# Optimization experiments

Hardware: AMD Instinct MI355X
Metric: run time of the kernel (lower is better)

Reference implementation:

```python
import jax, jax.numpy as jnp
import numpy as np

B, T, D, H = 2, 2048, 1024, 16
HS = D // H  # head_size = 64
EPS = 1e-5


def layer_norm(x, g, b):
    mu = jnp.mean(x, axis=-1, keepdims=True)
    var = jnp.var(x, axis=-1, keepdims=True)
    return (x - mu) * jax.lax.rsqrt(var + EPS) * g + b


def setup_inputs() -> dict:
    key = jax.random.key(0)
    ks = jax.random.split(key, 12)
    s_attn = 1.0 / np.sqrt(D)
    s_ff1 = 1.0 / np.sqrt(D)
    s_ff2 = 1.0 / np.sqrt(4 * D)
    return {
        "x": jax.random.normal(ks[0], (B, T, D), jnp.float32),
        "Wq": jax.random.normal(ks[1], (H, D, HS), jnp.float32) * s_attn,
        "Wk": jax.random.normal(ks[2], (H, D, HS), jnp.float32) * s_attn,
        "Wv": jax.random.normal(ks[3], (H, D, HS), jnp.float32) * s_attn,
        "Wo": jax.random.normal(ks[4], (H * HS, D), jnp.float32) * (1.0 / np.sqrt(H * HS)),
        "bo": jnp.zeros((D,), jnp.float32),
        "W1": jax.random.normal(ks[5], (D, 4 * D), jnp.float32) * s_ff1,
        "b1": jnp.zeros((4 * D,), jnp.float32),
        "W2": jax.random.normal(ks[6], (4 * D, D), jnp.float32) * s_ff2,
        "b2": jnp.zeros((D,), jnp.float32),
        "ln1_g": jnp.ones((D,), jnp.float32),
        "ln1_b": jnp.zeros((D,), jnp.float32),
        "ln2_g": jnp.ones((D,), jnp.float32),
        "ln2_b": jnp.zeros((D,), jnp.float32),
    }


def reference(x, Wq, Wk, Wv, Wo, bo, W1, b1, W2, b2, ln1_g, ln1_b, ln2_g, ln2_b):
    # --- self-attention on ln1(x) ---
    h = layer_norm(x, ln1_g, ln1_b)
    Q = jnp.einsum('bsd,hdk->bhsk', h, Wq)
    K = jnp.einsum('bsd,hdk->bhsk', h, Wk)
    V = jnp.einsum('bsd,hdk->bhsk', h, Wv)
    scores = jnp.einsum('bhqk,bhsk->bhqs', Q, K) * (HS ** -0.5)
    attn = jax.nn.softmax(scores, axis=-1)  # [B,H,T,T] non-causal, as in source
    out = jnp.einsum('bhqs,bhsk->bhqk', attn, V)
    out = out.transpose(0, 2, 1, 3).reshape(B, T, H * HS)  # concat heads
    sa = out @ Wo + bo
    x = x + sa
    # --- feed-forward on ln2(x) ---
    h2 = layer_norm(x, ln2_g, ln2_b)
    ff = jax.nn.relu(h2 @ W1 + b1) @ W2 + b2
    return x + ff
```

## Files before the change

### kernel.cpp

```cpp
#include <hip/hip_runtime.h>
#include <cstdint>
#include <cmath>

typedef __bf16 bf16;
typedef __bf16 bf16x8 __attribute__((ext_vector_type(8)));
typedef __bf16 bf16x4 __attribute__((ext_vector_type(4)));
typedef __bf16 bf16x2 __attribute__((ext_vector_type(2)));
typedef float  f32x4  __attribute__((ext_vector_type(4)));

#define B_   2
#define T_   2048
#define D_   1024
#define H_   16
#define HS_  64
#define NTOK (B_ * T_)

typedef __attribute__((address_space(1))) uint8_t* gp1_t;
typedef __attribute__((address_space(3))) uint8_t* lp3_t;
__device__ __forceinline__ void gl_lds16(const void* g, void* l) {
    __builtin_amdgcn_global_load_lds((gp1_t)(uintptr_t)g,
                                     (lp3_t)(uint32_t)(uintptr_t)l,
                                     16, 0, 0);
}

__device__ __forceinline__ f32x4 mfma16(bf16x8 a, bf16x8 b, f32x4 c) {
    return __builtin_amdgcn_mfma_f32_16x16x32_bf16(a, b, c, 0, 0, 0);
}

__device__ __forceinline__ uint32_t pk2(float lo, float hi) {
    bf16x2 t; t[0] = (bf16)lo; t[1] = (bf16)hi;
    return __builtin_bit_cast(uint32_t, t);
}
__device__ __forceinline__ void pl32(uint32_t& a, uint32_t& b) {
    asm("v_permlane32_swap_b32 %0, %1" : "+v"(a), "+v"(b));
}
__device__ __forceinline__ void pl16(uint32_t& a, uint32_t& b) {
    asm("v_permlane16_swap_b32 %0, %1" : "+v"(a), "+v"(b));
}

__global__ void tcast(const float* __restrict__ in, bf16* __restrict__ out,
                      int R, int C) {
    __shared__ float t[32][33];
    const int c0 = blockIdx.x * 32, r0 = blockIdx.y * 32;
    for (int i = 0; i < 4; i++) {
        int r = threadIdx.y + i * 8;
        t[r][threadIdx.x] = in[(size_t)(r0 + r) * C + c0 + threadIdx.x];
    }
    __syncthreads();
    for (int i = 0; i < 4; i++) {
        int rr = threadIdx.y + i * 8;
        out[(size_t)(c0 + rr) * R + r0 + threadIdx.x] = (bf16)t[threadIdx.x][rr];
    }
}

__global__ void qkv_pack(const float* __restrict__ Wq, const float* __restrict__ Wk,
                         const float* __restrict__ Wv, bf16* __restrict__ out) {
    const int z = blockIdx.z;
    const int qkv = z >> 4;
    const float* in = (qkv == 0 ? Wq : qkv == 1 ? Wk : Wv) + (size_t)(z & 15) * D_ * HS_;
    bf16* o = out + (size_t)z * HS_ * D_;
    __shared__ float t[32][33];
    const int c0 = blockIdx.x * 32, r0 = blockIdx.y * 32;
    for (int i = 0; i < 4; i++) {
        int r = threadIdx.y + i * 8;
        t[r][threadIdx.x] = in[(size_t)(r0 + r) * HS_ + c0 + threadIdx.x];
    }
    __syncthreads();
    for (int i = 0; i < 4; i++) {
        int rr = threadIdx.y + i * 8;
        o[(size_t)(c0 + rr) * D_ + r0 + threadIdx.x] = (bf16)t[threadIdx.x][rr];
    }
}

__global__ __launch_bounds__(256) void ln_kernel(const float* __restrict__ x,
                                                 const float* __restrict__ g,
                                                 const float* __restrict__ b,
                                                 bf16* __restrict__ out) {
    const int row = blockIdx.x;
    const int tid = threadIdx.x;
    const float4 v = ((const float4*)(x + (size_t)row * 1024))[tid];
    float s  = v.x + v.y + v.z + v.w;
    float s2 = v.x * v.x + v.y * v.y + v.z * v.z + v.w * v.w;
    for (int m = 1; m < 64; m <<= 1) {
        s  += __shfl_xor(s, m);
        s2 += __shfl_xor(s2, m);
    }
    __shared__ float rs[4], rq[4];
    const int lane = tid & 63, wv = tid >> 6;
    if (lane == 0) { rs[wv] = s; rq[wv] = s2; }
    __syncthreads();
    s  = rs[0] + rs[1] + rs[2] + rs[3];
    s2 = rq[0] + rq[1] + rq[2] + rq[3];
    const float mu   = s * (1.f / 1024.f);
    const float var  = s2 * (1.f / 1024.f) - mu * mu;
    const float rstd = rsqrtf(var + 1e-5f);
    const float4 gg = ((const float4*)g)[tid];
    const float4 bb = ((const float4*)b)[tid];
    bf16x4 o;
    o[0] = (bf16)((v.x - mu) * rstd * gg.x + bb.x);
    o[1] = (bf16)((v.y - mu) * rstd * gg.y + bb.y);
    o[2] = (bf16)((v.z - mu) * rstd * gg.z + bb.z);
    o[3] = (bf16)((v.w - mu) * rstd * gg.w + bb.w);
    *(bf16x4*)(out + (size_t)row * 1024 + tid * 4) = o;
}

__global__ __launch_bounds__(256) void combine4(const float* __restrict__ p0,
                                                const float* __restrict__ p1,
                                                const float* __restrict__ p2,
                                                const float* __restrict__ p3,
                                                const float* __restrict__ resid,
                                                const float* __restrict__ bias,
                                                float* __restrict__ out) {
    const int i4 = blockIdx.x * 256 + threadIdx.x;
    const float4 a = ((const float4*)p0)[i4];
    const float4 b = ((const float4*)p1)[i4];
    const float4 c = ((const float4*)p2)[i4];
    const float4 d = ((const float4*)p3)[i4];
    const float4 r = ((const float4*)resid)[i4];
    const float4 bb = ((const float4*)bias)[i4 & 255];
    float4 o;
    o.x = a.x + b.x + c.x + d.x + r.x + bb.x;
    o.y = a.y + b.y + c.y + d.y + r.y + bb.y;
    o.z = a.z + b.z + c.z + d.z + r.z + bb.z;
    o.w = a.w + b.w + c.w + d.w + r.w + bb.w;
    ((float4*)out)[i4] = o;
}

template <int BIAS, int RELU, int RES, int OUTBF16>
__global__ __launch_bounds__(256, 2) void gemm_bt(
    const bf16* __restrict__ A, const bf16* __restrict__ Bt,
    const float* __restrict__ bias, const float* __restrict__ resid,
    void* __restrict__ Cout, int M, int N, int K) {
    __shared__ __align__(16) bf16 As[2][128 * 32];
    __shared__ __align__(16) bf16 Bs[2][128 * 32];
    const int tid  = threadIdx.x;
    const int lane = tid & 63, w = tid >> 6;
    const int quad = lane >> 4, l15 = lane & 15;
    const int m0 = blockIdx.y * 128, n0 = blockIdx.x * 128;
    const int wm = (w & 1) * 64, wn = (w >> 1) * 64;

    f32x4 acc[4][4];
    for (int i = 0; i < 4; i++)
        for (int j = 0; j < 4; j++) acc[i][j] = f32x4{0.f, 0.f, 0.f, 0.f};

    const int arow = lane >> 2;
    const int acol = (lane & 3) * 8;
    const int c0 = w * 2, c1 = w * 2 + 1;

    for (int kt = 0; kt < K; kt += 64) {
        gl_lds16(A  + (size_t)(m0 + c0 * 16 + arow) * K + kt + acol,      &As[0][c0 * 512]);
        gl_lds16(A  + (size_t)(m0 + c1 * 16 + arow) * K + kt + acol,      &As[0][c1 * 512]);
        gl_lds16(A  + (size_t)(m0 + c0 * 16 + arow) * K + kt + 32 + acol, &As[1][c0 * 512]);
        gl_lds16(A  + (size_t)(m0 + c1 * 16 + arow) * K + kt + 32 + acol, &As[1][c1 * 512]);
        gl_lds16(Bt + (size_t)(n0 + c0 * 16 + arow) * K + kt + acol,      &Bs[0][c0 * 512]);
        gl_lds16(Bt + (size_t)(n0 + c1 * 16 + arow) * K + kt + acol,      &Bs[0][c1 * 512]);
        gl_lds16(Bt + (size_t)(n0 + c0 * 16 + arow) * K + kt + 32 + acol, &Bs[1][c0 * 512]);
        gl_lds16(Bt + (size_t)(n0 + c1 * 16 + arow) * K + kt + 32 + acol, &Bs[1][c1 * 512]);
        __syncthreads();
        for (int kh = 0; kh < 2; kh++) {
            bf16x8 af[4], bfr[4];
            for (int mi = 0; mi < 4; mi++)
                af[mi] = *(const bf16x8*)&As[kh][(wm + mi * 16 + l15) * 32 + quad * 8];
            for (int ni = 0; ni < 4; ni++)
                bfr[ni] = *(const bf16x8*)&Bs[kh][(wn + ni * 16 + l15) * 32 + quad * 8];
            for (int mi = 0; mi < 4; mi++)
                for (int ni = 0; ni < 4; ni++)
                    acc[mi][ni] = mfma16(af[mi], bfr[ni], acc[mi][ni]);
        }
        __syncthreads();
    }

    for (int mi = 0; mi < 4; mi++) {
        for (int ni = 0; ni < 4; ni++) {
            const int colb = n0 + wn + ni * 16 + l15;
            const float bv = BIAS ? bias[colb] : 0.f;
            for (int r = 0; r < 4; r++) {
                const int row = m0 + wm + mi * 16 + quad * 4 + r;
                float v = acc[mi][ni][r] + bv;
                if (RELU) v = fmaxf(v, 0.f);
                if (RES)  v += resid[(size_t)row * N + colb];
                if (OUTBF16) ((bf16*)Cout)[(size_t)row * N + colb] = (bf16)v;
                else         ((float*)Cout)[(size_t)row * N + colb] = v;
            }
        }
    }
}

template <int BIAS, int RELU, int VTP, int PARTIAL>
__global__ __launch_bounds__(512, 2) void gemm256(
    const bf16* __restrict__ A, const bf16* __restrict__ Bt,
    const float* __restrict__ bias, void* __restrict__ Cout,
    bf16* __restrict__ Vt, float* __restrict__ P0, float* __restrict__ P1,
    int M, int N, int K) {
    __shared__ __align__(16) bf16 Asub[4][256 * 32];
    __shared__ __align__(16) bf16 Bsub[4][256 * 32];
    const int tid  = threadIdx.x;
    const int lane = tid & 63, w = tid >> 6;
    const int wr = w >> 2, wc = w & 3;
    const int quad = lane >> 4, l15 = lane & 15;
    const int m0 = blockIdx.y * 256, n0 = blockIdx.x * 256;
    const int kpb = PARTIAL ? (K / (int)gridDim.z) : K;
    const int k0  = PARTIAL ? (int)blockIdx.z * kpb : 0;
    const int S   = kpb / 32;

    const int slog = (((lane & 3) ^ ((lane >> 3) & 3)) * 8);
    const int crow = lane >> 2;
    const bf16* gA0 = A  + (size_t)(m0 + 32 * w + crow)      * K + k0 + slog;
    const bf16* gA1 = A  + (size_t)(m0 + 32 * w + 16 + crow) * K + k0 + slog;
    const bf16* gB0 = Bt + (size_t)(n0 + 32 * w + crow)      * K + k0 + slog;
    const bf16* gB1 = Bt + (size_t)(n0 + 32 * w + 16 + crow) * K + k0 + slog;

    for (int t = 0; t < 3; t++) {
        gl_lds16(gA0, &Asub[t][(32 * w) * 32]);
        gl_lds16(gA1, &Asub[t][(32 * w + 16) * 32]);
        gl_lds16(gB0, &Bsub[t][(32 * w) * 32]);
        gl_lds16(gB1, &Bsub[t][(32 * w + 16) * 32]);
        gA0 += 32; gA1 += 32; gB0 += 32; gB1 += 32;
    }

    f32x4 acc[8][4];
#pragma unroll
    for (int i = 0; i < 8; i++)
#pragma unroll
        for (int j = 0; j < 4; j++) acc[i][j] = f32x4{0.f, 0.f, 0.f, 0.f};

    const int swz = (quad ^ ((l15 >> 1) & 3)) * 8;
    const int aof = (wr * 128 + l15) * 32 + swz;
    const int bof = (wc * 64 + l15) * 32 + swz;

    asm volatile("s_waitcnt vmcnt(8)" ::: "memory");
    __builtin_amdgcn_sched_barrier(0);
    __builtin_amdgcn_s_barrier();

    for (int s = 0; s < S; s++) {
        const bf16* Ab = &Asub[s & 3][0];
        const bf16* Bb = &Bsub[s & 3][0];
        const int pb = (s + 3) & 3;
        bf16x8 af[4], bfr[4];
#pragma unroll
        for (int f = 0; f < 4; f++) af[f] = *(const bf16x8*)&Ab[aof + f * 512];
#pragma unroll
        for (int n = 0; n < 4; n++) bfr[n] = *(const bf16x8*)&Bb[bof + n * 512];
        if (s + 3 < S) {
            gl_lds16(gA0, &Asub[pb][(32 * w) * 32]);
            gl_lds16(gA1, &Asub[pb][(32 * w + 16) * 32]);
            gA0 += 32; gA1 += 32;
        }
        __builtin_amdgcn_sched_barrier(0);
        __builtin_amdgcn_s_barrier();
        asm volatile("s_waitcnt lgkmcnt(0)" ::: "memory");
        __builtin_amdgcn_sched_barrier(0);
        __builtin_amdgcn_s_setprio(1);
#pragma unroll
        for (int f = 0; f < 4; f++)
#pragma unroll
            for (int n = 0; n < 4; n++)
                acc[f][n] = mfma16(af[f], bfr[n], acc[f][n]);
        __builtin_amdgcn_s_setprio(0);
        __builtin_amdgcn_sched_barrier(0);
        __builtin_amdgcn_s_barrier();
#pragma unroll
        for (int f = 0; f < 4; f++) af[f] = *(const bf16x8*)&Ab[aof + 2048 + f * 512];
        if (s + 3 < S) {
            gl_lds16(gB0, &Bsub[pb][(32 * w) * 32]);
            gl_lds16(gB1, &Bsub[pb][(32 * w + 16) * 32]);
            gB0 += 32; gB1 += 32;
        }
        __builtin_amdgcn_sched_barrier(0);
        __builtin_amdgcn_s_barrier();
        asm volatile("s_waitcnt lgkmcnt(0)" ::: "memory");
        __builtin_amdgcn_sched_barrier(0);
        __builtin_amdgcn_s_setprio(1);
#pragma unroll
        for (int f = 0; f < 4; f++)
#pragma unroll
            for (int n = 0; n < 4; n++)
                acc[4 + f][n] = mfma16(af[f], bfr[n], acc[4 + f][n]);
        __builtin_amdgcn_s_setprio(0);
        __builtin_amdgcn_sched_barrier(0);
        if (s <= S - 4)      asm volatile("s_waitcnt vmcnt(8)" ::: "memory");
        else if (s == S - 3) asm volatile("s_waitcnt vmcnt(4)" ::: "memory");
        else if (s == S - 2) asm volatile("s_waitcnt vmcnt(0)" ::: "memory");
        __builtin_amdgcn_s_barrier();
    }

#pragma unroll
    for (int mi = 0; mi < 8; mi++) {
#pragma unroll
        for (int ni = 0; ni < 4; ni++) {
            const int colb = n0 + wc * 64 + ni * 16 + l15;
            const int row0 = m0 + wr * 128 + (mi >> 2) * 64 + (mi & 3) * 16 + quad * 4;
            if (VTP && colb >= 2048) {
                const int h = (colb - 2048) >> 6, hs = (colb - 2048) & 63;
                const int b = row0 >> 11;
                bf16x4 p4;
                p4[0] = (bf16)acc[mi][ni][0];
                p4[1] = (bf16)acc[mi][ni][1];
                p4[2] = (bf16)acc[mi][ni][2];
                p4[3] = (bf16)acc[mi][ni][3];
                *(bf16x4*)&Vt[((size_t)(b * 16 + h) * 64 + hs) * T_ + (row0 & 2047)] = p4;
                continue;
            }
            if (PARTIAL) {
                float* Cz = ((int)blockIdx.z < 2 ? P0 : P1) + (size_t)(blockIdx.z & 1) * M * N;
                for (int r = 0; r < 4; r++)
                    Cz[(size_t)(row0 + r) * N + colb] = acc[mi][ni][r];
            } else {
                const float bv = BIAS ? bias[colb] : 0.f;
                for (int r = 0; r < 4; r++) {
                    float v = acc[mi][ni][r] + bv;
                    if (RELU) v = fmaxf(v, 0.f);
                    ((bf16*)Cout)[(size_t)(row0 + r) * N + colb] = (bf16)v;
                }
            }
        }
    }
}

#define LSTR 68
#define NJ   (T_ / 64)
__global__ __launch_bounds__(256, 2) void flash_attn(const bf16* __restrict__ QKV,
                                                     const bf16* __restrict__ Vt,
                                                     bf16* __restrict__ attn_out) {
    const int bh = blockIdx.y, b = bh >> 4, h = bh & 15;
    const int q0 = blockIdx.x * 128;
    const int tid = threadIdx.x, lane = tid & 63, w = tid >> 6;
    const int quad = lane >> 4, l15 = lane & 15;
    __shared__ __align__(16) bf16 Ks[2][64 * LSTR];
    __shared__ __align__(16) bf16 Vs[2][64 * LSTR];
    const bf16* Qb = QKV + (size_t)b * T_ * 3072 + h * 64;
    const bf16* Kb = QKV + (size_t)b * T_ * 3072 + 1024 + h * 64;
    const bf16* Vb = Vt  + (size_t)bh * HS_ * T_;

    const float sc = 0.125f * 1.44269504088896f;
    const int sr = tid >> 2, scc = (tid & 3) * 16;

    bf16x8 QA[2][2];
    for (int qnt = 0; qnt < 2; qnt++) {
        const size_t row = (size_t)(q0 + w * 32 + qnt * 16 + l15) * 3072;
        for (int kk = 0; kk < 2; kk++) {
            bf16x8 q = *(const bf16x8*)&Qb[row + kk * 32 + quad * 8];
            for (int i = 0; i < 8; i++) q[i] = (bf16)((float)q[i] * sc);
            QA[qnt][kk] = q;
        }
    }

    bf16x8 ones8;
    for (int i = 0; i < 8; i++) ones8[i] = (bf16)1.0f;

    f32x4 O[2][4], lacc[2];
    for (int mi = 0; mi < 2; mi++) {
        lacc[mi] = f32x4{0.f, 0.f, 0.f, 0.f};
        for (int n = 0; n < 4; n++) O[mi][n] = f32x4{0.f, 0.f, 0.f, 0.f};
    }

    *(bf16x8*)&Ks[0][sr * LSTR + scc]     = *(const bf16x8*)&Kb[(size_t)sr * 3072 + scc];
    *(bf16x8*)&Ks[0][sr * LSTR + scc + 8] = *(const bf16x8*)&Kb[(size_t)sr * 3072 + scc + 8];
    *(bf16x8*)&Vs[0][sr * LSTR + scc]     = *(const bf16x8*)&Vb[(size_t)sr * T_ + scc];
    *(bf16x8*)&Vs[0][sr * LSTR + scc + 8] = *(const bf16x8*)&Vb[(size_t)sr * T_ + scc + 8];
    __syncthreads();

    bf16x8 k0, k1, v0, v1;
    for (int j = 0; j < NJ; j++) {
        const int buf = j & 1;
        if (j + 1 < NJ) {
            const int s1 = (j + 1) * 64;
            k0 = *(const bf16x8*)&Kb[(size_t)(s1 + sr) * 3072 + scc];
            k1 = *(const bf16x8*)&Kb[(size_t)(s1 + sr) * 3072 + scc + 8];
            v0 = *(const bf16x8*)&Vb[(size_t)sr * T_ + s1 + scc];
            v1 = *(const bf16x8*)&Vb[(size_t)sr * T_ + s1 + scc + 8];
        }
        bf16x8 KB[4][2];
#pragma unroll
        for (int smt = 0; smt < 4; smt++)
#pragma unroll
            for (int kk = 0; kk < 2; kk++)
                KB[smt][kk] = *(const bf16x8*)&Ks[buf][(smt * 16 + l15) * LSTR + kk * 32 + quad * 8];

        bf16x8 PA[2][2];
#pragma unroll
        for (int qnt = 0; qnt < 2; qnt++) {
            f32x4 ST[4];
#pragma unroll
            for (int smt = 0; smt < 4; smt++) ST[smt] = f32x4{0.f, 0.f, 0.f, 0.f};
            __builtin_amdgcn_s_setprio(1);
#pragma unroll
            for (int kk = 0; kk < 2; kk++)
#pragma unroll
                for (int smt = 0; smt < 4; smt++)
                    ST[smt] = mfma16(KB[smt][kk], QA[qnt][kk], ST[smt]);
            __builtin_amdgcn_s_setprio(0);
            uint32_t w00 = pk2(__builtin_amdgcn_exp2f(ST[0][0]), __builtin_amdgcn_exp2f(ST[0][1]));
            uint32_t w01 = pk2(__builtin_amdgcn_exp2f(ST[0][2]), __builtin_amdgcn_exp2f(ST[0][3]));
            uint32_t w10 = pk2(__builtin_amdgcn_exp2f(ST[1][0]), __builtin_amdgcn_exp2f(ST[1][1]));
            uint32_t w11 = pk2(__builtin_amdgcn_exp2f(ST[1][2]), __builtin_amdgcn_exp2f(ST[1][3]));
            uint32_t w20 = pk2(__builtin_amdgcn_exp2f(ST[2][0]), __builtin_amdgcn_exp2f(ST[2][1]));
            uint32_t w21 = pk2(__builtin_amdgcn_exp2f(ST[2][2]), __builtin_amdgcn_exp2f(ST[2][3]));
            uint32_t w30 = pk2(__builtin_amdgcn_exp2f(ST[3][0]), __builtin_amdgcn_exp2f(ST[3][1]));
            uint32_t w31 = pk2(__builtin_amdgcn_exp2f(ST[3][2]), __builtin_amdgcn_exp2f(ST[3][3]));
            pl32(w00, w10); pl16(w00, w10);
            pl32(w01, w11); pl16(w01, w11);
            pl32(w20, w30); pl16(w20, w30);
            pl32(w21, w31); pl16(w21, w31);
            union { uint32_t u[4]; bf16x8 v; } pa0, pa1;
            pa0.u[0] = w00; pa0.u[1] = w01; pa0.u[2] = w10; pa0.u[3] = w11;
            pa1.u[0] = w20; pa1.u[1] = w21; pa1.u[2] = w30; pa1.u[3] = w31;
            PA[qnt][0] = pa0.v;
            PA[qnt][1] = pa1.v;
        }
        bf16x8 VB[4][2];
#pragma unroll
        for (int n = 0; n < 4; n++)
#pragma unroll
            for (int kk = 0; kk < 2; kk++)
                VB[n][kk] = *(const bf16x8*)&Vs[buf][(n * 16 + l15) * LSTR + kk * 32 + quad * 8];
        __builtin_amdgcn_s_setprio(1);
#pragma unroll
        for (int mi = 0; mi < 2; mi++) {
            const bf16x8 PA0 = PA[mi][0];
            const bf16x8 PA1 = PA[mi][1];
#pragma unroll
            for (int n = 0; n < 4; n++) {
                O[mi][n] = mfma16(PA0, VB[n][0], O[mi][n]);
                O[mi][n] = mfma16(PA1, VB[n][1], O[mi][n]);
            }
            lacc[mi] = mfma16(PA0, ones8, lacc[mi]);
            lacc[mi] = mfma16(PA1, ones8, lacc[mi]);
        }
        __builtin_amdgcn_s_setprio(0);
        if (j + 1 < NJ) {
            *(bf16x8*)&Ks[buf ^ 1][sr * LSTR + scc]     = k0;
            *(bf16x8*)&Ks[buf ^ 1][sr * LSTR + scc + 8] = k1;
            *(bf16x8*)&Vs[buf ^ 1][sr * LSTR + scc]     = v0;
            *(bf16x8*)&Vs[buf ^ 1][sr * LSTR + scc + 8] = v1;
        }
        __syncthreads();
    }

    for (int mi = 0; mi < 2; mi++) {
        for (int r = 0; r < 4; r++) {
            const float inv = 1.f / lacc[mi][r];
            const size_t tok = (size_t)b * T_ + q0 + w * 32 + mi * 16 + quad * 4 + r;
            for (int n = 0; n < 4; n++)
                attn_out[tok * 1024 + h * 64 + n * 16 + l15] = (bf16)(O[mi][n][r] * inv);
        }
    }
}

extern "C" void kernel_launch(void* const* d_in, const int* in_sizes, int n_in,
                              void* d_out, int out_size, void* d_ws, size_t ws_size,
                              hipStream_t stream) {
    const float* x   = (const float*)d_in[0];
    const float* Wq  = (const float*)d_in[1];
    const float* Wk  = (const float*)d_in[2];
    const float* Wv  = (const float*)d_in[3];
    const float* Wo  = (const float*)d_in[4];
    const float* bo  = (const float*)d_in[5];
    const float* W1  = (const float*)d_in[6];
    const float* b1  = (const float*)d_in[7];
    const float* W2  = (const float*)d_in[8];
    const float* b2  = (const float*)d_in[9];
    const float* g1  = (const float*)d_in[10];
    const float* be1 = (const float*)d_in[11];
    const float* g2  = (const float*)d_in[12];
    const float* be2 = (const float*)d_in[13];

    char* ws = (char*)d_ws;
    const size_t MB = 1ull << 20;
    bf16*  WqkvT = (bf16*)(ws);
    bf16*  WoT   = (bf16*)(ws + 6  * MB);
    bf16*  W1T   = (bf16*)(ws + 8  * MB);
    bf16*  W2T   = (bf16*)(ws + 16 * MB);
    bf16*  hbuf  = (bf16*)(ws + 24 * MB);
    bf16*  QKV   = (bf16*)(ws + 32 * MB);
    bf16*  Vt    = (bf16*)(ws + 56 * MB);
    bf16*  attn  = (bf16*)(ws + 64 * MB);
    float* x2    = (float*)(ws + 72 * MB);
    bf16*  ff1   = (bf16*)(ws + 32 * MB);
    float* partA = (float*)(ws);
    float* partB = (float*)(ws + 88 * MB);
    float* out   = (float*)d_out;

    dim3 tb(32, 8);
    qkv_pack<<<dim3(2, 32, 48), tb, 0, stream>>>(Wq, Wk, Wv, WqkvT);
    tcast<<<dim3(32, 32),  tb, 0, stream>>>(Wo, WoT, 1024, 1024);
    tcast<<<dim3(128, 32), tb, 0, stream>>>(W1, W1T, 1024, 4096);
    tcast<<<dim3(32, 128), tb, 0, stream>>>(W2, W2T, 4096, 1024);
    ln_kernel<<<NTOK, 256, 0, stream>>>(x, g1, be1, hbuf);
    gemm256<0, 0, 1, 0><<<dim3(12, 16), 512, 0, stream>>>(
        hbuf, WqkvT, nullptr, QKV, Vt, nullptr, nullptr, NTOK, 3072, 1024);
    flash_attn<<<dim3(T_ / 128, B_ * H_), 256, 0, stream>>>(QKV, Vt, attn);
    gemm_bt<1, 0, 1, 0><<<dim3(8, 32), 256, 0, stream>>>(attn, WoT, bo, x, x2, NTOK, 1024, 1024);
    ln_kernel<<<NTOK, 256, 0, stream>>>(x2, g2, be2, hbuf);
    gemm256<1, 1, 0, 0><<<dim3(16, 16), 512, 0, stream>>>(
        hbuf, W1T, b1, ff1, nullptr, nullptr, nullptr, NTOK, 4096, 1024);
    gemm256<0, 0, 0, 1><<<dim3(4, 16, 4), 512, 0, stream>>>(
        ff1, W2T, nullptr, nullptr, nullptr, partA, partB, NTOK, 1024, 4096);
    combine4<<<NTOK, 256, 0, stream>>>(partA, partA + (size_t)NTOK * 1024,
                                       partB, partB + (size_t)NTOK * 1024,
                                       x2, b2, out);
}
```

Measured before the change: 341.1 us.

## Make flash attention single-wave with register-direct K/V loads; use 128-tile QKV GEMM

Flash attention drops shared-memory K/V staging and block barriers. Each 64-thread block now handles 32 queries and loads K and V fragments straight from global memory into registers, prefetching the next tile while the current one is computed. The QKV projection moves from the 256-tile GEMM to the 128-tile gemm_bt, which gains a V-transpose epilogue, giving more blocks. The aim is to remove LDS traffic and sync stalls and raise block count, at the cost of each wave re-reading K/V from global memory/L2 with less reuse across waves.

```diff
diff --git a/kernel.cpp b/kernel.cpp
--- a/kernel.cpp
+++ b/kernel.cpp
@@ -126,11 +126,11 @@
     ((float4*)out)[i4] = o;
 }
 
-template <int BIAS, int RELU, int RES, int OUTBF16>
+template <int BIAS, int RELU, int RES, int OUTBF16, int VTP = 0>
 __global__ __launch_bounds__(256, 2) void gemm_bt(
     const bf16* __restrict__ A, const bf16* __restrict__ Bt,
     const float* __restrict__ bias, const float* __restrict__ resid,
-    void* __restrict__ Cout, int M, int N, int K) {
+    void* __restrict__ Cout, bf16* __restrict__ Vt, int M, int N, int K) {
     __shared__ __align__(16) bf16 As[2][128 * 32];
     __shared__ __align__(16) bf16 Bs[2][128 * 32];
     const int tid  = threadIdx.x;
@@ -173,6 +173,18 @@
     for (int mi = 0; mi < 4; mi++) {
         for (int ni = 0; ni < 4; ni++) {
             const int colb = n0 + wn + ni * 16 + l15;
+            if (VTP && colb >= 2048) {
+                const int h = (colb - 2048) >> 6, hs = (colb - 2048) & 63;
+                const int row0 = m0 + wm + mi * 16 + quad * 4;
+                const int b = row0 >> 11;
+                bf16x4 p4;
+                p4[0] = (bf16)acc[mi][ni][0];
+                p4[1] = (bf16)acc[mi][ni][1];
+                p4[2] = (bf16)acc[mi][ni][2];
+                p4[3] = (bf16)acc[mi][ni][3];
+                *(bf16x4*)&Vt[((size_t)(b * 16 + h) * 64 + hs) * T_ + (row0 & 2047)] = p4;
+                continue;
+            }
             const float bv = BIAS ? bias[colb] : 0.f;
             for (int r = 0; r < 4; r++) {
                 const int row = m0 + wm + mi * 16 + quad * 4 + r;
@@ -317,29 +329,28 @@
     }
 }
 
-#define LSTR 68
 #define NJ   (T_ / 64)
-__global__ __launch_bounds__(256, 2) void flash_attn(const bf16* __restrict__ QKV,
-                                                     const bf16* __restrict__ Vt,
-                                                     bf16* __restrict__ attn_out) {
+__global__ __launch_bounds__(64, 2) void flash_attn(const bf16* __restrict__ QKV,
+                                                    const bf16* __restrict__ Vt,
+                                                    bf16* __restrict__ attn_out) {
     const int bh = blockIdx.y, b = bh >> 4, h = bh & 15;
-    const int q0 = blockIdx.x * 128;
-    const int tid = threadIdx.x, lane = tid & 63, w = tid >> 6;
+    const int q0 = blockIdx.x * 32;
+    const int lane = threadIdx.x;
     const int quad = lane >> 4, l15 = lane & 15;
-    __shared__ __align__(16) bf16 Ks[2][64 * LSTR];
-    __shared__ __align__(16) bf16 Vs[2][64 * LSTR];
     const bf16* Qb = QKV + (size_t)b * T_ * 3072 + h * 64;
     const bf16* Kb = QKV + (size_t)b * T_ * 3072 + 1024 + h * 64;
     const bf16* Vb = Vt  + (size_t)bh * HS_ * T_;
 
     const float sc = 0.125f * 1.44269504088896f;
-    const int sr = tid >> 2, scc = (tid & 3) * 16;
+    const int koff = quad * 8;
 
     bf16x8 QA[2][2];
+#pragma unroll
     for (int qnt = 0; qnt < 2; qnt++) {
-        const size_t row = (size_t)(q0 + w * 32 + qnt * 16 + l15) * 3072;
+        const size_t row = (size_t)(q0 + qnt * 16 + l15) * 3072;
+#pragma unroll
         for (int kk = 0; kk < 2; kk++) {
-            bf16x8 q = *(const bf16x8*)&Qb[row + kk * 32 + quad * 8];
+            bf16x8 q = *(const bf16x8*)&Qb[row + kk * 32 + koff];
             for (int i = 0; i < 8; i++) q[i] = (bf16)((float)q[i] * sc);
             QA[qnt][kk] = q;
         }
@@ -349,55 +360,58 @@
     for (int i = 0; i < 8; i++) ones8[i] = (bf16)1.0f;
 
     f32x4 O[2][4], lacc[2];
+#pragma unroll
     for (int mi = 0; mi < 2; mi++) {
         lacc[mi] = f32x4{0.f, 0.f, 0.f, 0.f};
         for (int n = 0; n < 4; n++) O[mi][n] = f32x4{0.f, 0.f, 0.f, 0.f};
     }
 
-    *(bf16x8*)&Ks[0][sr * LSTR + scc]     = *(const bf16x8*)&Kb[(size_t)sr * 3072 + scc];
-    *(bf16x8*)&Ks[0][sr * LSTR + scc + 8] = *(const bf16x8*)&Kb[(size_t)sr * 3072 + scc + 8];
-    *(bf16x8*)&Vs[0][sr * LSTR + scc]     = *(const bf16x8*)&Vb[(size_t)sr * T_ + scc];
-    *(bf16x8*)&Vs[0][sr * LSTR + scc + 8] = *(const bf16x8*)&Vb[(size_t)sr * T_ + scc + 8];
-    __syncthreads();
-
-    bf16x8 k0, k1, v0, v1;
+    bf16x8 KB[4][2], VB[4][2];
+#pragma unroll
+    for (int smt = 0; smt < 4; smt++)
+#pragma unroll
+        for (int kk = 0; kk < 2; kk++)
+            KB[smt][kk] = *(const bf16x8*)&Kb[(size_t)(smt * 16 + l15) * 3072 + kk * 32 + koff];
+#pragma unroll
+    for (int n = 0; n < 4; n++)
+#pragma unroll
+        for (int kk = 0; kk < 2; kk++)
+            VB[n][kk] = *(const bf16x8*)&Vb[(size_t)(n * 16 + l15) * T_ + kk * 32 + koff];
+
     for (int j = 0; j < NJ; j++) {
-        const int buf = j & 1;
+        f32x4 ST[2][4];
+#pragma unroll
+        for (int qnt = 0; qnt < 2; qnt++)
+#pragma unroll
+            for (int smt = 0; smt < 4; smt++) ST[qnt][smt] = f32x4{0.f, 0.f, 0.f, 0.f};
+        __builtin_amdgcn_s_setprio(1);
+#pragma unroll
+        for (int kk = 0; kk < 2; kk++)
+#pragma unroll
+            for (int qnt = 0; qnt < 2; qnt++)
+#pragma unroll
+                for (int smt = 0; smt < 4; smt++)
+                    ST[qnt][smt] = mfma16(KB[smt][kk], QA[qnt][kk], ST[qnt][smt]);
+        __builtin_amdgcn_s_setprio(0);
         if (j + 1 < NJ) {
-            const int s1 = (j + 1) * 64;
-            k0 = *(const bf16x8*)&Kb[(size_t)(s1 + sr) * 3072 + scc];
-            k1 = *(const bf16x8*)&Kb[(size_t)(s1 + sr) * 3072 + scc + 8];
-            v0 = *(const bf16x8*)&Vb[(size_t)sr * T_ + s1 + scc];
-            v1 = *(const bf16x8*)&Vb[(size_t)sr * T_ + s1 + scc + 8];
-        }
-        bf16x8 KB[4][2];
-#pragma unroll
-        for (int smt = 0; smt < 4; smt++)
-#pragma unroll
-            for (int kk = 0; kk < 2; kk++)
-                KB[smt][kk] = *(const bf16x8*)&Ks[buf][(smt * 16 + l15) * LSTR + kk * 32 + quad * 8];
-
+            const size_t s1 = (size_t)(j + 1) * 64;
+#pragma unroll
+            for (int smt = 0; smt < 4; smt++)
+#pragma unroll
+                for (int kk = 0; kk < 2; kk++)
+                    KB[smt][kk] = *(const bf16x8*)&Kb[(s1 + smt * 16 + l15) * 3072 + kk * 32 + koff];
+        }
         bf16x8 PA[2][2];
 #pragma unroll
         for (int qnt = 0; qnt < 2; qnt++) {
-            f32x4 ST[4];
-#pragma unroll
-            for (int smt = 0; smt < 4; smt++) ST[smt] = f32x4{0.f, 0.f, 0.f, 0.f};
-            __builtin_amdgcn_s_setprio(1);
-#pragma unroll
-            for (int kk = 0; kk < 2; kk++)
-#pragma unroll
-                for (int smt = 0; smt < 4; smt++)
-                    ST[smt] = mfma16(KB[smt][kk], QA[qnt][kk], ST[smt]);
-            __builtin_amdgcn_s_setprio(0);
-            uint32_t w00 = pk2(__builtin_amdgcn_exp2f(ST[0][0]), __builtin_amdgcn_exp2f(ST[0][1]));
-            uint32_t w01 = pk2(__builtin_amdgcn_exp2f(ST[0][2]), __builtin_amdgcn_exp2f(ST[0][3]));
-            uint32_t w10 = pk2(__builtin_amdgcn_exp2f(ST[1][0]), __builtin_amdgcn_exp2f(ST[1][1]));
-            uint32_t w11 = pk2(__builtin_amdgcn_exp2f(ST[1][2]), __builtin_amdgcn_exp2f(ST[1][3]));
-            uint32_t w20 = pk2(__builtin_amdgcn_exp2f(ST[2][0]), __builtin_amdgcn_exp2f(ST[2][1]));
-            uint32_t w21 = pk2(__builtin_amdgcn_exp2f(ST[2][2]), __builtin_amdgcn_exp2f(ST[2][3]));
-            uint32_t w30 = pk2(__builtin_amdgcn_exp2f(ST[3][0]), __builtin_amdgcn_exp2f(ST[3][1]));
-            uint32_t w31 = pk2(__builtin_amdgcn_exp2f(ST[3][2]), __builtin_amdgcn_exp2f(ST[3][3]));
+            uint32_t w00 = pk2(__builtin_amdgcn_exp2f(ST[qnt][0][0]), __builtin_amdgcn_exp2f(ST[qnt][0][1]));
+            uint32_t w01 = pk2(__builtin_amdgcn_exp2f(ST[qnt][0][2]), __builtin_amdgcn_exp2f(ST[qnt][0][3]));
+            uint32_t w10 = pk2(__builtin_amdgcn_exp2f(ST[qnt][1][0]), __builtin_amdgcn_exp2f(ST[qnt][1][1]));
+            uint32_t w11 = pk2(__builtin_amdgcn_exp2f(ST[qnt][1][2]), __builtin_amdgcn_exp2f(ST[qnt][1][3]));
+            uint32_t w20 = pk2(__builtin_amdgcn_exp2f(ST[qnt][2][0]), __builtin_amdgcn_exp2f(ST[qnt][2][1]));
+            uint32_t w21 = pk2(__builtin_amdgcn_exp2f(ST[qnt][2][2]), __builtin_amdgcn_exp2f(ST[qnt][2][3]));
+            uint32_t w30 = pk2(__builtin_amdgcn_exp2f(ST[qnt][3][0]), __builtin_amdgcn_exp2f(ST[qnt][3][1]));
+            uint32_t w31 = pk2(__builtin_amdgcn_exp2f(ST[qnt][3][2]), __builtin_amdgcn_exp2f(ST[qnt][3][3]));
             pl32(w00, w10); pl16(w00, w10);
             pl32(w01, w11); pl16(w01, w11);
             pl32(w20, w30); pl16(w20, w30);
@@ -408,12 +422,6 @@
             PA[qnt][0] = pa0.v;
             PA[qnt][1] = pa1.v;
         }
-        bf16x8 VB[4][2];
-#pragma unroll
-        for (int n = 0; n < 4; n++)
-#pragma unroll
-            for (int kk = 0; kk < 2; kk++)
-                VB[n][kk] = *(const bf16x8*)&Vs[buf][(n * 16 + l15) * LSTR + kk * 32 + quad * 8];
         __builtin_amdgcn_s_setprio(1);
 #pragma unroll
         for (int mi = 0; mi < 2; mi++) {
@@ -429,18 +437,20 @@
         }
         __builtin_amdgcn_s_setprio(0);
         if (j + 1 < NJ) {
-            *(bf16x8*)&Ks[buf ^ 1][sr * LSTR + scc]     = k0;
-            *(bf16x8*)&Ks[buf ^ 1][sr * LSTR + scc + 8] = k1;
-            *(bf16x8*)&Vs[buf ^ 1][sr * LSTR + scc]     = v0;
-            *(bf16x8*)&Vs[buf ^ 1][sr * LSTR + scc + 8] = v1;
-        }
-        __syncthreads();
-    }
-
+            const int s1 = (j + 1) * 64;
+#pragma unroll
+            for (int n = 0; n < 4; n++)
+#pragma unroll
+                for (int kk = 0; kk < 2; kk++)
+                    VB[n][kk] = *(const bf16x8*)&Vb[(size_t)(n * 16 + l15) * T_ + s1 + kk * 32 + koff];
+        }
+    }
+
+#pragma unroll
     for (int mi = 0; mi < 2; mi++) {
         for (int r = 0; r < 4; r++) {
             const float inv = 1.f / lacc[mi][r];
-            const size_t tok = (size_t)b * T_ + q0 + w * 32 + mi * 16 + quad * 4 + r;
+            const size_t tok = (size_t)b * T_ + q0 + mi * 16 + quad * 4 + r;
             for (int n = 0; n < 4; n++)
                 attn_out[tok * 1024 + h * 64 + n * 16 + l15] = (bf16)(O[mi][n][r] * inv);
         }
@@ -487,10 +497,11 @@
     tcast<<<dim3(128, 32), tb, 0, stream>>>(W1, W1T, 1024, 4096);
     tcast<<<dim3(32, 128), tb, 0, stream>>>(W2, W2T, 4096, 1024);
     ln_kernel<<<NTOK, 256, 0, stream>>>(x, g1, be1, hbuf);
-    gemm256<0, 0, 1, 0><<<dim3(12, 16), 512, 0, stream>>>(
-        hbuf, WqkvT, nullptr, QKV, Vt, nullptr, nullptr, NTOK, 3072, 1024);
-    flash_attn<<<dim3(T_ / 128, B_ * H_), 256, 0, stream>>>(QKV, Vt, attn);
-    gemm_bt<1, 0, 1, 0><<<dim3(8, 32), 256, 0, stream>>>(attn, WoT, bo, x, x2, NTOK, 1024, 1024);
+    gemm_bt<0, 0, 0, 1, 1><<<dim3(24, 32), 256, 0, stream>>>(
+        hbuf, WqkvT, nullptr, nullptr, QKV, Vt, NTOK, 3072, 1024);
+    flash_attn<<<dim3(T_ / 32, B_ * H_), 64, 0, stream>>>(QKV, Vt, attn);
+    gemm_bt<1, 0, 1, 0><<<dim3(8, 32), 256, 0, stream>>>(
+        attn, WoT, bo, x, x2, nullptr, NTOK, 1024, 1024);
     ln_kernel<<<NTOK, 256, 0, stream>>>(x2, g2, be2, hbuf);
     gemm256<1, 1, 0, 0><<<dim3(16, 16), 512, 0, stream>>>(
         hbuf, W1T, b1, ff1, nullptr, nullptr, nullptr, NTOK, 4096, 1024);
```

Result: slower. 411.2 us (+20.6%).

## Use 512-thread flash attention blocks with one 16-row query tile per wave

Applied to the files above, without the earlier changes.

Flash attention blocks grow from 4 to 8 waves, and each wave now handles 16 query rows instead of 32, so the 128-row block tile is kept. Per-thread register state drops (QA, O and lacc are halved) and the launch bounds target higher occupancy. K/V tile loads are spread across 512 threads, one 16-byte load each. In exchange, every K/V LDS fragment is read by twice as many waves for the same MFMA work, and each barrier now synchronises more waves.

```diff
diff --git a/kernel.cpp b/kernel.cpp
--- a/kernel.cpp
+++ b/kernel.cpp
@@ -319,7 +319,7 @@
 
 #define LSTR 68
 #define NJ   (T_ / 64)
-__global__ __launch_bounds__(256, 2) void flash_attn(const bf16* __restrict__ QKV,
+__global__ __launch_bounds__(512, 4) void flash_attn(const bf16* __restrict__ QKV,
                                                      const bf16* __restrict__ Vt,
                                                      bf16* __restrict__ attn_out) {
     const int bh = blockIdx.y, b = bh >> 4, h = bh & 15;
@@ -333,42 +333,38 @@
     const bf16* Vb = Vt  + (size_t)bh * HS_ * T_;
 
     const float sc = 0.125f * 1.44269504088896f;
-    const int sr = tid >> 2, scc = (tid & 3) * 16;
-
-    bf16x8 QA[2][2];
-    for (int qnt = 0; qnt < 2; qnt++) {
-        const size_t row = (size_t)(q0 + w * 32 + qnt * 16 + l15) * 3072;
+    const int sr = tid >> 3, scc = (tid & 7) * 8;
+
+    bf16x8 QA[2];
+    {
+        const size_t row = (size_t)(q0 + w * 16 + l15) * 3072;
+#pragma unroll
         for (int kk = 0; kk < 2; kk++) {
             bf16x8 q = *(const bf16x8*)&Qb[row + kk * 32 + quad * 8];
             for (int i = 0; i < 8; i++) q[i] = (bf16)((float)q[i] * sc);
-            QA[qnt][kk] = q;
+            QA[kk] = q;
         }
     }
 
     bf16x8 ones8;
     for (int i = 0; i < 8; i++) ones8[i] = (bf16)1.0f;
 
-    f32x4 O[2][4], lacc[2];
-    for (int mi = 0; mi < 2; mi++) {
-        lacc[mi] = f32x4{0.f, 0.f, 0.f, 0.f};
-        for (int n = 0; n < 4; n++) O[mi][n] = f32x4{0.f, 0.f, 0.f, 0.f};
-    }
-
-    *(bf16x8*)&Ks[0][sr * LSTR + scc]     = *(const bf16x8*)&Kb[(size_t)sr * 3072 + scc];
-    *(bf16x8*)&Ks[0][sr * LSTR + scc + 8] = *(const bf16x8*)&Kb[(size_t)sr * 3072 + scc + 8];
-    *(bf16x8*)&Vs[0][sr * LSTR + scc]     = *(const bf16x8*)&Vb[(size_t)sr * T_ + scc];
-    *(bf16x8*)&Vs[0][sr * LSTR + scc + 8] = *(const bf16x8*)&Vb[(size_t)sr * T_ + scc + 8];
+    f32x4 O[4], lacc;
+    lacc = f32x4{0.f, 0.f, 0.f, 0.f};
+#pragma unroll
+    for (int n = 0; n < 4; n++) O[n] = f32x4{0.f, 0.f, 0.f, 0.f};
+
+    *(bf16x8*)&Ks[0][sr * LSTR + scc] = *(const bf16x8*)&Kb[(size_t)sr * 3072 + scc];
+    *(bf16x8*)&Vs[0][sr * LSTR + scc] = *(const bf16x8*)&Vb[(size_t)sr * T_ + scc];
     __syncthreads();
 
-    bf16x8 k0, k1, v0, v1;
+    bf16x8 kpre, vpre;
     for (int j = 0; j < NJ; j++) {
         const int buf = j & 1;
         if (j + 1 < NJ) {
             const int s1 = (j + 1) * 64;
-            k0 = *(const bf16x8*)&Kb[(size_t)(s1 + sr) * 3072 + scc];
-            k1 = *(const bf16x8*)&Kb[(size_t)(s1 + sr) * 3072 + scc + 8];
-            v0 = *(const bf16x8*)&Vb[(size_t)sr * T_ + s1 + scc];
-            v1 = *(const bf16x8*)&Vb[(size_t)sr * T_ + s1 + scc + 8];
+            kpre = *(const bf16x8*)&Kb[(size_t)(s1 + sr) * 3072 + scc];
+            vpre = *(const bf16x8*)&Vb[(size_t)sr * T_ + s1 + scc];
         }
         bf16x8 KB[4][2];
 #pragma unroll
@@ -377,19 +373,19 @@
             for (int kk = 0; kk < 2; kk++)
                 KB[smt][kk] = *(const bf16x8*)&Ks[buf][(smt * 16 + l15) * LSTR + kk * 32 + quad * 8];
 
-        bf16x8 PA[2][2];
-#pragma unroll
-        for (int qnt = 0; qnt < 2; qnt++) {
-            f32x4 ST[4];
-#pragma unroll
-            for (int smt = 0; smt < 4; smt++) ST[smt] = f32x4{0.f, 0.f, 0.f, 0.f};
-            __builtin_amdgcn_s_setprio(1);
-#pragma unroll
-            for (int kk = 0; kk < 2; kk++)
-#pragma unroll
-                for (int smt = 0; smt < 4; smt++)
-                    ST[smt] = mfma16(KB[smt][kk], QA[qnt][kk], ST[smt]);
-            __builtin_amdgcn_s_setprio(0);
+        f32x4 ST[4];
+#pragma unroll
+        for (int smt = 0; smt < 4; smt++) ST[smt] = f32x4{0.f, 0.f, 0.f, 0.f};
+        __builtin_amdgcn_s_setprio(1);
+#pragma unroll
+        for (int kk = 0; kk < 2; kk++)
+#pragma unroll
+            for (int smt = 0; smt < 4; smt++)
+                ST[smt] = mfma16(KB[smt][kk], QA[kk], ST[smt]);
+        __builtin_amdgcn_s_setprio(0);
+
+        bf16x8 PA0v, PA1v;
+        {
             uint32_t w00 = pk2(__builtin_amdgcn_exp2f(ST[0][0]), __builtin_amdgcn_exp2f(ST[0][1]));
             uint32_t w01 = pk2(__builtin_amdgcn_exp2f(ST[0][2]), __builtin_amdgcn_exp2f(ST[0][3]));
             uint32_t w10 = pk2(__builtin_amdgcn_exp2f(ST[1][0]), __builtin_amdgcn_exp2f(ST[1][1]));
@@ -405,45 +401,39 @@
             union { uint32_t u[4]; bf16x8 v; } pa0, pa1;
             pa0.u[0] = w00; pa0.u[1] = w01; pa0.u[2] = w10; pa0.u[3] = w11;
             pa1.u[0] = w20; pa1.u[1] = w21; pa1.u[2] = w30; pa1.u[3] = w31;
-            PA[qnt][0] = pa0.v;
-            PA[qnt][1] = pa1.v;
-        }
+            PA0v = pa0.v;
+            PA1v = pa1.v;
+        }
+
         bf16x8 VB[4][2];
 #pragma unroll
         for (int n = 0; n < 4; n++)
 #pragma unroll
             for (int kk = 0; kk < 2; kk++)
                 VB[n][kk] = *(const bf16x8*)&Vs[buf][(n * 16 + l15) * LSTR + kk * 32 + quad * 8];
+
         __builtin_amdgcn_s_setprio(1);
 #pragma unroll
-        for (int mi = 0; mi < 2; mi++) {
-            const bf16x8 PA0 = PA[mi][0];
-            const bf16x8 PA1 = PA[mi][1];
-#pragma unroll
-            for (int n = 0; n < 4; n++) {
-                O[mi][n] = mfma16(PA0, VB[n][0], O[mi][n]);
-                O[mi][n] = mfma16(PA1, VB[n][1], O[mi][n]);
-            }
-            lacc[mi] = mfma16(PA0, ones8, lacc[mi]);
-            lacc[mi] = mfma16(PA1, ones8, lacc[mi]);
-        }
+        for (int n = 0; n < 4; n++) {
+            O[n] = mfma16(PA0v, VB[n][0], O[n]);
+            O[n] = mfma16(PA1v, VB[n][1], O[n]);
+        }
+        lacc = mfma16(PA0v, ones8, lacc);
+        lacc = mfma16(PA1v, ones8, lacc);
         __builtin_amdgcn_s_setprio(0);
+
         if (j + 1 < NJ) {
-            *(bf16x8*)&Ks[buf ^ 1][sr * LSTR + scc]     = k0;
-            *(bf16x8*)&Ks[buf ^ 1][sr * LSTR + scc + 8] = k1;
-            *(bf16x8*)&Vs[buf ^ 1][sr * LSTR + scc]     = v0;
-            *(bf16x8*)&Vs[buf ^ 1][sr * LSTR + scc + 8] = v1;
+            *(bf16x8*)&Ks[buf ^ 1][sr * LSTR + scc] = kpre;
+            *(bf16x8*)&Vs[buf ^ 1][sr * LSTR + scc] = vpre;
         }
         __syncthreads();
     }
 
-    for (int mi = 0; mi < 2; mi++) {
-        for (int r = 0; r < 4; r++) {
-            const float inv = 1.f / lacc[mi][r];
-            const size_t tok = (size_t)b * T_ + q0 + w * 32 + mi * 16 + quad * 4 + r;
-            for (int n = 0; n < 4; n++)
-                attn_out[tok * 1024 + h * 64 + n * 16 + l15] = (bf16)(O[mi][n][r] * inv);
-        }
+    for (int r = 0; r < 4; r++) {
+        const float inv = 1.f / lacc[r];
+        const size_t tok = (size_t)b * T_ + q0 + w * 16 + quad * 4 + r;
+        for (int n = 0; n < 4; n++)
+            attn_out[tok * 1024 + h * 64 + n * 16 + l15] = (bf16)(O[n][r] * inv);
     }
 }
 
@@ -489,8 +479,9 @@
     ln_kernel<<<NTOK, 256, 0, stream>>>(x, g1, be1, hbuf);
     gemm256<0, 0, 1, 0><<<dim3(12, 16), 512, 0, stream>>>(
         hbuf, WqkvT, nullptr, QKV, Vt, nullptr, nullptr, NTOK, 3072, 1024);
-    flash_attn<<<dim3(T_ / 128, B_ * H_), 256, 0, stream>>>(QKV, Vt, attn);
-    gemm_bt<1, 0, 1, 0><<<dim3(8, 32), 256, 0, stream>>>(attn, WoT, bo, x, x2, NTOK, 1024, 1024);
+    flash_attn<<<dim3(T_ / 128, B_ * H_), 512, 0, stream>>>(QKV, Vt, attn);
+    gemm_bt<1, 0, 1, 0><<<dim3(8, 32), 256, 0, stream>>>(
+        attn, WoT, bo, x, x2, NTOK, 1024, 1024);
     ln_kernel<<<NTOK, 256, 0, stream>>>(x2, g2, be2, hbuf);
     gemm256<1, 1, 0, 0><<<dim3(16, 16), 512, 0, stream>>>(
         hbuf, W1T, b1, ff1, nullptr, nullptr, nullptr, NTOK, 4096, 1024);
```

Result: slower. 356.0 us (+4.4%).

## Split flash attention KV range across two wave groups and merge in LDS

Applied to the files above, without the earlier changes.

Doubles the flash attention block to 512 threads, with each half of the waves processing half of the key/value sequence for the same 128 queries using separate double-buffered LDS tiles. At the end the second half writes its partial O and row sums into LDS and the first half adds them and normalizes. Because no running max is kept, the partials can be summed directly. The aim is more waves per CU and more latency hiding for the attention kernel, at the cost of double the LDS per block and an extra reduction step with a barrier.

```diff
diff --git a/kernel.cpp b/kernel.cpp
--- a/kernel.cpp
+++ b/kernel.cpp
@@ -318,26 +318,32 @@
 }
 
 #define LSTR 68
-#define NJ   (T_ / 64)
-__global__ __launch_bounds__(256, 2) void flash_attn(const bf16* __restrict__ QKV,
+#define NJH  (T_ / 2 / 64)
+__global__ __launch_bounds__(512, 4) void flash_attn(const bf16* __restrict__ QKV,
                                                      const bf16* __restrict__ Vt,
                                                      bf16* __restrict__ attn_out) {
     const int bh = blockIdx.y, b = bh >> 4, h = bh & 15;
     const int q0 = blockIdx.x * 128;
     const int tid = threadIdx.x, lane = tid & 63, w = tid >> 6;
+    const int hf = w >> 2, wl = w & 3;
     const int quad = lane >> 4, l15 = lane & 15;
-    __shared__ __align__(16) bf16 Ks[2][64 * LSTR];
-    __shared__ __align__(16) bf16 Vs[2][64 * LSTR];
+    __shared__ __align__(16) bf16 Ks[2][2][64 * LSTR];
+    __shared__ __align__(16) bf16 Vs[2][2][64 * LSTR];
     const bf16* Qb = QKV + (size_t)b * T_ * 3072 + h * 64;
     const bf16* Kb = QKV + (size_t)b * T_ * 3072 + 1024 + h * 64;
     const bf16* Vb = Vt  + (size_t)bh * HS_ * T_;
 
     const float sc = 0.125f * 1.44269504088896f;
-    const int sr = tid >> 2, scc = (tid & 3) * 16;
+    const int st  = tid & 255;
+    const int hfs = tid >> 8;
+    const int sr = st >> 2, scc = (st & 3) * 16;
+    const int kvbase = hfs * 1024;
 
     bf16x8 QA[2][2];
+#pragma unroll
     for (int qnt = 0; qnt < 2; qnt++) {
-        const size_t row = (size_t)(q0 + w * 32 + qnt * 16 + l15) * 3072;
+        const size_t row = (size_t)(q0 + wl * 32 + qnt * 16 + l15) * 3072;
+#pragma unroll
         for (int kk = 0; kk < 2; kk++) {
             bf16x8 q = *(const bf16x8*)&Qb[row + kk * 32 + quad * 8];
             for (int i = 0; i < 8; i++) q[i] = (bf16)((float)q[i] * sc);
@@ -349,22 +355,23 @@
     for (int i = 0; i < 8; i++) ones8[i] = (bf16)1.0f;
 
     f32x4 O[2][4], lacc[2];
+#pragma unroll
     for (int mi = 0; mi < 2; mi++) {
         lacc[mi] = f32x4{0.f, 0.f, 0.f, 0.f};
         for (int n = 0; n < 4; n++) O[mi][n] = f32x4{0.f, 0.f, 0.f, 0.f};
     }
 
-    *(bf16x8*)&Ks[0][sr * LSTR + scc]     = *(const bf16x8*)&Kb[(size_t)sr * 3072 + scc];
-    *(bf16x8*)&Ks[0][sr * LSTR + scc + 8] = *(const bf16x8*)&Kb[(size_t)sr * 3072 + scc + 8];
-    *(bf16x8*)&Vs[0][sr * LSTR + scc]     = *(const bf16x8*)&Vb[(size_t)sr * T_ + scc];
-    *(bf16x8*)&Vs[0][sr * LSTR + scc + 8] = *(const bf16x8*)&Vb[(size_t)sr * T_ + scc + 8];
+    *(bf16x8*)&Ks[hfs][0][sr * LSTR + scc]     = *(const bf16x8*)&Kb[(size_t)(kvbase + sr) * 3072 + scc];
+    *(bf16x8*)&Ks[hfs][0][sr * LSTR + scc + 8] = *(const bf16x8*)&Kb[(size_t)(kvbase + sr) * 3072 + scc + 8];
+    *(bf16x8*)&Vs[hfs][0][sr * LSTR + scc]     = *(const bf16x8*)&Vb[(size_t)sr * T_ + kvbase + scc];
+    *(bf16x8*)&Vs[hfs][0][sr * LSTR + scc + 8] = *(const bf16x8*)&Vb[(size_t)sr * T_ + kvbase + scc + 8];
     __syncthreads();
 
     bf16x8 k0, k1, v0, v1;
-    for (int j = 0; j < NJ; j++) {
+    for (int j = 0; j < NJH; j++) {
         const int buf = j & 1;
-        if (j + 1 < NJ) {
-            const int s1 = (j + 1) * 64;
+        if (j + 1 < NJH) {
+            const int s1 = kvbase + (j + 1) * 64;
             k0 = *(const bf16x8*)&Kb[(size_t)(s1 + sr) * 3072 + scc];
             k1 = *(const bf16x8*)&Kb[(size_t)(s1 + sr) * 3072 + scc + 8];
             v0 = *(const bf16x8*)&Vb[(size_t)sr * T_ + s1 + scc];
@@ -375,7 +382,7 @@
         for (int smt = 0; smt < 4; smt++)
 #pragma unroll
             for (int kk = 0; kk < 2; kk++)
-                KB[smt][kk] = *(const bf16x8*)&Ks[buf][(smt * 16 + l15) * LSTR + kk * 32 + quad * 8];
+                KB[smt][kk] = *(const bf16x8*)&Ks[hf][buf][(smt * 16 + l15) * LSTR + kk * 32 + quad * 8];
 
         bf16x8 PA[2][2];
 #pragma unroll
@@ -413,7 +420,7 @@
         for (int n = 0; n < 4; n++)
 #pragma unroll
             for (int kk = 0; kk < 2; kk++)
-                VB[n][kk] = *(const bf16x8*)&Vs[buf][(n * 16 + l15) * LSTR + kk * 32 + quad * 8];
+                VB[n][kk] = *(const bf16x8*)&Vs[hf][buf][(n * 16 + l15) * LSTR + kk * 32 + quad * 8];
         __builtin_amdgcn_s_setprio(1);
 #pragma unroll
         for (int mi = 0; mi < 2; mi++) {
@@ -428,21 +435,48 @@
             lacc[mi] = mfma16(PA1, ones8, lacc[mi]);
         }
         __builtin_amdgcn_s_setprio(0);
-        if (j + 1 < NJ) {
-            *(bf16x8*)&Ks[buf ^ 1][sr * LSTR + scc]     = k0;
-            *(bf16x8*)&Ks[buf ^ 1][sr * LSTR + scc + 8] = k1;
-            *(bf16x8*)&Vs[buf ^ 1][sr * LSTR + scc]     = v0;
-            *(bf16x8*)&Vs[buf ^ 1][sr * LSTR + scc + 8] = v1;
+        if (j + 1 < NJH) {
+            *(bf16x8*)&Ks[hfs][buf ^ 1][sr * LSTR + scc]     = k0;
+            *(bf16x8*)&Ks[hfs][buf ^ 1][sr * LSTR + scc + 8] = k1;
+            *(bf16x8*)&Vs[hfs][buf ^ 1][sr * LSTR + scc]     = v0;
+            *(bf16x8*)&Vs[hfs][buf ^ 1][sr * LSTR + scc + 8] = v1;
         }
         __syncthreads();
     }
 
-    for (int mi = 0; mi < 2; mi++) {
-        for (int r = 0; r < 4; r++) {
-            const float inv = 1.f / lacc[mi][r];
-            const size_t tok = (size_t)b * T_ + q0 + w * 32 + mi * 16 + quad * 4 + r;
-            for (int n = 0; n < 4; n++)
-                attn_out[tok * 1024 + h * 64 + n * 16 + l15] = (bf16)(O[mi][n][r] * inv);
+    f32x4* cbO = (f32x4*)&Ks[0][0][0];
+    f32x4* cbL = (f32x4*)&Vs[0][0][0];
+    const int slot = wl * 64 + lane;
+    if (hf == 1) {
+#pragma unroll
+        for (int mi = 0; mi < 2; mi++)
+#pragma unroll
+            for (int n = 0; n < 4; n++) cbO[slot * 8 + mi * 4 + n] = O[mi][n];
+        cbL[slot * 2 + 0] = lacc[0];
+        cbL[slot * 2 + 1] = lacc[1];
+    }
+    __syncthreads();
+    if (hf == 0) {
+#pragma unroll
+        for (int mi = 0; mi < 2; mi++) {
+#pragma unroll
+            for (int n = 0; n < 4; n++) {
+                const f32x4 p = cbO[slot * 8 + mi * 4 + n];
+                O[mi][n][0] += p[0]; O[mi][n][1] += p[1];
+                O[mi][n][2] += p[2]; O[mi][n][3] += p[3];
+            }
+            const f32x4 pl = cbL[slot * 2 + mi];
+            lacc[mi][0] += pl[0]; lacc[mi][1] += pl[1];
+            lacc[mi][2] += pl[2]; lacc[mi][3] += pl[3];
+        }
+#pragma unroll
+        for (int mi = 0; mi < 2; mi++) {
+            for (int r = 0; r < 4; r++) {
+                const float inv = 1.f / lacc[mi][r];
+                const size_t tok = (size_t)b * T_ + q0 + wl * 32 + mi * 16 + quad * 4 + r;
+                for (int n = 0; n < 4; n++)
+                    attn_out[tok * 1024 + h * 64 + n * 16 + l15] = (bf16)(O[mi][n][r] * inv);
+            }
         }
     }
 }
@@ -489,8 +523,9 @@
     ln_kernel<<<NTOK, 256, 0, stream>>>(x, g1, be1, hbuf);
     gemm256<0, 0, 1, 0><<<dim3(12, 16), 512, 0, stream>>>(
         hbuf, WqkvT, nullptr, QKV, Vt, nullptr, nullptr, NTOK, 3072, 1024);
-    flash_attn<<<dim3(T_ / 128, B_ * H_), 256, 0, stream>>>(QKV, Vt, attn);
-    gemm_bt<1, 0, 1, 0><<<dim3(8, 32), 256, 0, stream>>>(attn, WoT, bo, x, x2, NTOK, 1024, 1024);
+    flash_attn<<<dim3(T_ / 128, B_ * H_), 512, 0, stream>>>(QKV, Vt, attn);
+    gemm_bt<1, 0, 1, 0><<<dim3(8, 32), 256, 0, stream>>>(
+        attn, WoT, bo, x, x2, NTOK, 1024, 1024);
     ln_kernel<<<NTOK, 256, 0, stream>>>(x2, g2, be2, hbuf);
     gemm256<1, 1, 0, 0><<<dim3(16, 16), 512, 0, stream>>>(
         hbuf, W1T, b1, ff1, nullptr, nullptr, nullptr, NTOK, 4096, 1024);
```

Measured after the change: 348.4 us. 2.1% more time.
